# Kernel optimization log

Measured on AMD Instinct MI355X. Metric: run time of the kernel, lower is better.

The kernel has to match this reference:

```python
import jax, jax.numpy as jnp
import numpy as np

IN, H = 512, 1024
EPS = 1e-5

def _ln(x, g, b):
    mu = jnp.mean(x, axis=-1, keepdims=True)
    var = jnp.mean(jnp.square(x - mu), axis=-1, keepdims=True)
    return (x - mu) * jax.lax.rsqrt(var + EPS) * g + b

def setup_inputs() -> dict:
    key = jax.random.key(0)
    ks = jax.random.split(key, 8)
    B = 8192
    x = jax.random.normal(ks[0], (B, IN), jnp.float32)
    h_prev = jax.random.normal(ks[1], (B, H), jnp.float32)
    c_prev = jax.random.normal(ks[2], (B, H), jnp.float32)
    # Xavier-uniform weights (torch Linear: weight [out, in])
    lim_i = float(np.sqrt(6.0 / (IN + 4 * H)))
    lim_h = float(np.sqrt(6.0 / (H + 4 * H)))
    Wi = jax.random.uniform(ks[3], (4 * H, IN), jnp.float32, -lim_i, lim_i)
    Wh = jax.random.uniform(ks[4], (4 * H, H), jnp.float32, -lim_h, lim_h)
    # biases zero-ish with forget-gate slice set to 1.0 (matches _initialize_weights)
    bi = jnp.zeros((4 * H,), jnp.float32).at[H:2 * H].set(1.0)
    bh = jnp.zeros((4 * H,), jnp.float32).at[H:2 * H].set(1.0)
    g_in = jnp.ones((4 * H,), jnp.float32); b_in = jnp.zeros((4 * H,), jnp.float32)
    g_hid = jnp.ones((4 * H,), jnp.float32); b_hid = jnp.zeros((4 * H,), jnp.float32)
    g_cell = jnp.ones((H,), jnp.float32); b_cell = jnp.zeros((H,), jnp.float32)
    return {"x": x, "h_prev": h_prev, "c_prev": c_prev,
            "Wi": Wi, "bi": bi, "Wh": Wh, "bh": bh,
            "g_in": g_in, "b_in": b_in, "g_hid": g_hid, "b_hid": b_hid,
            "g_cell": g_cell, "b_cell": b_cell}

def reference(x, h_prev, c_prev, Wi, bi, Wh, bh, g_in, b_in, g_hid, b_hid, g_cell, b_cell):
    input_proj = _ln(x @ Wi.T + bi, g_in, b_in)          # [B, 4H]
    hidden_proj = _ln(h_prev @ Wh.T + bh, g_hid, b_hid)  # [B, 4H]
    combined = input_proj + hidden_proj
    i, f, g, o = jnp.split(combined, 4, axis=1)
    i = jax.nn.sigmoid(i); f = jax.nn.sigmoid(f)
    g = jnp.tanh(g); o = jax.nn.sigmoid(o)
    c_new = f * c_prev + i * g
    h_new = o * jnp.tanh(_ln(c_new, g_cell, b_cell))
    return (h_new, c_new)
```

## Files before the change

kernel.cpp:

```cpp
#include <hip/hip_runtime.h>
#include <hip/hip_bf16.h>

#define EPS 1e-5f

typedef __attribute__((ext_vector_type(8))) short short8;
typedef __attribute__((ext_vector_type(4))) short short4v;
typedef __attribute__((ext_vector_type(4))) float floatx4;

__device__ inline float b2f(short s) {
    union { unsigned u; float f; } v;
    v.u = ((unsigned)(unsigned short)s) << 16;
    return v.f;
}
__device__ inline float sigmoidf_(float x) { return 1.f / (1.f + __expf(-x)); }
__device__ inline float tanhf_(float x) { return 1.f - 2.f / (__expf(2.f * x) + 1.f); }

__device__ inline void load_lds16(const void* g, void* l) {
    __builtin_amdgcn_global_load_lds(
        (const __attribute__((address_space(1))) void*)g,
        (__attribute__((address_space(3))) void*)l, 16, 0, 0);
}

__global__ __launch_bounds__(256)
void cvt_bf16(const float* __restrict__ s0, __hip_bfloat16* __restrict__ d0, int n0_,
              const float* __restrict__ s1, __hip_bfloat16* __restrict__ d1, int n1_,
              const float* __restrict__ s2, __hip_bfloat16* __restrict__ d2, int n2_,
              const float* __restrict__ s3, __hip_bfloat16* __restrict__ d3, int n3_) {
    const float* s; __hip_bfloat16* d; int n;
    switch (blockIdx.y) {
        case 0:  s = s0; d = d0; n = n0_; break;
        case 1:  s = s1; d = d1; n = n1_; break;
        case 2:  s = s2; d = d2; n = n2_; break;
        default: s = s3; d = d3; n = n3_; break;
    }
    const int idx = (blockIdx.x * 256 + threadIdx.x) * 4;
    if (idx < n) {
        float4 v = *(const float4*)(s + idx);
        union { short4v sv; __hip_bfloat16 h[4]; } u;
        u.h[0] = __float2bfloat16(v.x); u.h[1] = __float2bfloat16(v.y);
        u.h[2] = __float2bfloat16(v.z); u.h[3] = __float2bfloat16(v.w);
        *(short4v*)(d + idx) = u.sv;
    }
}

__global__ __launch_bounds__(256, 3)
void gemm_bf16(const __hip_bfloat16* __restrict__ A, const __hip_bfloat16* __restrict__ W,
               const float* __restrict__ bias, __hip_bfloat16* __restrict__ out, int K) {
    __shared__ alignas(16) __hip_bfloat16 smem[17408];
    __hip_bfloat16* sA = smem;
    __hip_bfloat16* sB = smem + 8192;

    const int t    = threadIdx.x;
    const int lane = t & 63;
    const int wave = t >> 6;
    const int quad = lane >> 4;
    const int rl   = lane & 15;
    const int wm   = (wave >> 1) * 64;
    const int wn   = (wave & 1) * 64;
    const int m0   = blockIdx.y * 128;
    const int n0   = blockIdx.x * 128;

    floatx4 acc[4][4];
    #pragma unroll
    for (int i = 0; i < 4; ++i)
        #pragma unroll
        for (int j = 0; j < 4; ++j)
            acc[i][j] = (floatx4){0.f, 0.f, 0.f, 0.f};

    int srow[4], scol[4];
    #pragma unroll
    for (int i = 0; i < 4; ++i) {
        const int cl  = (wave * 4 + i) * 64 + lane;
        const int row = cl >> 3;
        srow[i] = row;
        scol[i] = ((cl & 7) ^ (row & 7)) * 8;
    }

    for (int k0 = 0; k0 < K; k0 += 64) {
        __syncthreads();
        #pragma unroll
        for (int i = 0; i < 4; ++i) {
            load_lds16(A + (size_t)(m0 + srow[i]) * K + k0 + scol[i], sA + (wave * 4 + i) * 512);
            load_lds16(W + (size_t)(n0 + srow[i]) * K + k0 + scol[i], sB + (wave * 4 + i) * 512);
        }
        __syncthreads();
        #pragma unroll
        for (int kk = 0; kk < 2; ++kk) {
            short8 aF[4], bF[4];
            #pragma unroll
            for (int i = 0; i < 4; ++i) {
                const int r = wm + i * 16 + rl;
                const int c = kk * 4 + quad;
                aF[i] = *(const short8*)(sA + (r * 8 + (c ^ (r & 7))) * 8);
            }
            #pragma unroll
            for (int j = 0; j < 4; ++j) {
                const int r = wn + j * 16 + rl;
                const int c = kk * 4 + quad;
                bF[j] = *(const short8*)(sB + (r * 8 + (c ^ (r & 7))) * 8);
            }
            #pragma unroll
            for (int i = 0; i < 4; ++i)
                #pragma unroll
                for (int j = 0; j < 4; ++j)
                    acc[i][j] = __builtin_amdgcn_mfma_f32_16x16x32_bf16(aF[i], bF[j], acc[i][j], 0, 0, 0);
        }
    }

    __syncthreads();
    #pragma unroll
    for (int j = 0; j < 4; ++j) {
        const int col = wn + j * 16 + rl;
        const float bv = bias[n0 + col];
        #pragma unroll
        for (int i = 0; i < 4; ++i) {
            const int rbase = wm + i * 16 + quad * 4;
            #pragma unroll
            for (int r = 0; r < 4; ++r)
                smem[(rbase + r) * 136 + col] = __float2bfloat16(acc[i][j][r] + bv);
        }
    }
    __syncthreads();
    #pragma unroll
    for (int p = 0; p < 8; ++p) {
        const int ch  = p * 256 + t;
        const int row = ch >> 4;
        const int c8  = (ch & 15) * 8;
        short8 v = *(const short8*)(smem + row * 136 + c8);
        *(short8*)(out + (size_t)(m0 + row) * 4096 + n0 + c8) = v;
    }
}

__device__ inline void red4(float& a, float& b, float& c, float& d, float* sred) {
    #pragma unroll
    for (int off = 32; off > 0; off >>= 1) {
        a += __shfl_down(a, off); b += __shfl_down(b, off);
        c += __shfl_down(c, off); d += __shfl_down(d, off);
    }
    const int w = threadIdx.x >> 6;
    if ((threadIdx.x & 63) == 0) {
        sred[w] = a; sred[w + 4] = b; sred[w + 8] = c; sred[w + 12] = d;
    }
    __syncthreads();
    a = sred[0] + sred[1] + sred[2] + sred[3];
    b = sred[4] + sred[5] + sred[6] + sred[7];
    c = sred[8] + sred[9] + sred[10] + sred[11];
    d = sred[12] + sred[13] + sred[14] + sred[15];
    __syncthreads();
}

__device__ inline void red2(float& a, float& b, float* sred) {
    #pragma unroll
    for (int off = 32; off > 0; off >>= 1) {
        a += __shfl_down(a, off); b += __shfl_down(b, off);
    }
    const int w = threadIdx.x >> 6;
    if ((threadIdx.x & 63) == 0) { sred[w] = a; sred[w + 4] = b; }
    __syncthreads();
    a = sred[0] + sred[1] + sred[2] + sred[3];
    b = sred[4] + sred[5] + sred[6] + sred[7];
    __syncthreads();
}

__global__ __launch_bounds__(256)
void ln_gates(const __hip_bfloat16* __restrict__ Pi, const __hip_bfloat16* __restrict__ Ph,
              const float* __restrict__ c_prev,
              const float* __restrict__ g_in, const float* __restrict__ b_in,
              const float* __restrict__ g_hid, const float* __restrict__ b_hid,
              const float* __restrict__ g_cell, const float* __restrict__ b_cell,
              float* __restrict__ h_out, float* __restrict__ c_out) {
    const int row = blockIdx.x;
    const int t   = threadIdx.x;
    __shared__ float sred[16];

    const __hip_bfloat16* pi = Pi + (size_t)row * 4096;
    const __hip_bfloat16* ph = Ph + (size_t)row * 4096;

    float si = 0.f, sqi = 0.f, sh = 0.f, sqh = 0.f;
    #pragma unroll
    for (int it = 0; it < 2; ++it) {
        const int s = t + it * 256;
        short8 vi = *(const short8*)(pi + s * 8);
        short8 vh = *(const short8*)(ph + s * 8);
        #pragma unroll
        for (int e = 0; e < 8; ++e) {
            float f = b2f(vi[e]); si += f; sqi += f * f;
            float g = b2f(vh[e]); sh += g; sqh += g * g;
        }
    }
    red4(si, sqi, sh, sqh, sred);
    const float mu_i = si * (1.f / 4096.f);
    const float rs_i = rsqrtf(sqi * (1.f / 4096.f) - mu_i * mu_i + EPS);
    const float mu_h = sh * (1.f / 4096.f);
    const float rs_h = rsqrtf(sqh * (1.f / 4096.f) - mu_h * mu_h + EPS);

    const int j0 = t * 4;
    float comb[4][4];
    #pragma unroll
    for (int gidx = 0; gidx < 4; ++gidx) {
        const int col = gidx * 1024 + j0;
        short4v vi = *(const short4v*)(pi + col);
        short4v vh = *(const short4v*)(ph + col);
        floatx4 gi  = *(const floatx4*)(g_in  + col);
        floatx4 bii = *(const floatx4*)(b_in  + col);
        floatx4 gh  = *(const floatx4*)(g_hid + col);
        floatx4 bhh = *(const floatx4*)(b_hid + col);
        #pragma unroll
        for (int e = 0; e < 4; ++e)
            comb[gidx][e] = (b2f(vi[e]) - mu_i) * rs_i * gi[e] + bii[e]
                          + (b2f(vh[e]) - mu_h) * rs_h * gh[e] + bhh[e];
    }

    floatx4 cp = *(const floatx4*)(c_prev + (size_t)row * 1024 + j0);
    float cn[4], ov[4];
    float sc = 0.f, scq = 0.f;
    #pragma unroll
    for (int e = 0; e < 4; ++e) {
        const float iv = sigmoidf_(comb[0][e]);
        const float fv = sigmoidf_(comb[1][e]);
        const float gv = tanhf_(comb[2][e]);
        ov[e] = sigmoidf_(comb[3][e]);
        const float c = fv * cp[e] + iv * gv;
        cn[e] = c; sc += c; scq += c * c;
    }
    red2(sc, scq, sred);
    const float mu_c = sc * (1.f / 1024.f);
    const float rs_c = rsqrtf(scq * (1.f / 1024.f) - mu_c * mu_c + EPS);

    floatx4 gc = *(const floatx4*)(g_cell + j0);
    floatx4 bc = *(const floatx4*)(b_cell + j0);
    floatx4 hv, cv;
    #pragma unroll
    for (int e = 0; e < 4; ++e) {
        const float nc = (cn[e] - mu_c) * rs_c * gc[e] + bc[e];
        hv[e] = ov[e] * tanhf_(nc);
        cv[e] = cn[e];
    }
    *(floatx4*)(h_out + (size_t)row * 1024 + j0) = hv;
    *(floatx4*)(c_out + (size_t)row * 1024 + j0) = cv;
}

extern "C" void kernel_launch(void* const* d_in, const int* in_sizes, int n_in,
                              void* d_out, int out_size, void* d_ws, size_t ws_size,
                              hipStream_t stream) {
    const float* x      = (const float*)d_in[0];
    const float* h_prev = (const float*)d_in[1];
    const float* c_prev = (const float*)d_in[2];
    const float* Wi     = (const float*)d_in[3];
    const float* bi     = (const float*)d_in[4];
    const float* Wh     = (const float*)d_in[5];
    const float* bh     = (const float*)d_in[6];
    const float* g_in   = (const float*)d_in[7];
    const float* b_in   = (const float*)d_in[8];
    const float* g_hid  = (const float*)d_in[9];
    const float* b_hid  = (const float*)d_in[10];
    const float* g_cell = (const float*)d_in[11];
    const float* b_cell = (const float*)d_in[12];

    __hip_bfloat16* Pi = (__hip_bfloat16*)d_ws;
    __hip_bfloat16* Ph = Pi + (size_t)8192 * 4096;

    const int NX = 8192 * 512, NH = 8192 * 1024, NWI = 4096 * 512, NWH = 4096 * 1024;
    __hip_bfloat16* xb  = (__hip_bfloat16*)d_out;
    __hip_bfloat16* hb  = xb + NX;
    __hip_bfloat16* Wib = hb + NH;
    __hip_bfloat16* Whb = Wib + NWI;

    float* h_out = (float*)d_out;
    float* c_out = h_out + (size_t)8192 * 1024;

    hipLaunchKernelGGL(cvt_bf16, dim3(8192, 4), dim3(256), 0, stream,
                       x, xb, NX, h_prev, hb, NH, Wi, Wib, NWI, Wh, Whb, NWH);

    dim3 grid(32, 64), blk(256);
    hipLaunchKernelGGL(gemm_bf16, grid, blk, 0, stream, xb, Wib, bi, Pi, 512);
    hipLaunchKernelGGL(gemm_bf16, grid, blk, 0, stream, hb, Whb, bh, Ph, 1024);
    hipLaunchKernelGGL(ln_gates, dim3(8192), blk, 0, stream, Pi, Ph, c_prev,
                       g_in, b_in, g_hid, b_hid, g_cell, b_cell, h_out, c_out);
}
```

Baseline: 340.6 us.

## Fuse LayerNorm row statistics into GEMM epilogue to skip a reduction pass

The GEMM epilogue now computes per-row partial sums and sums of squares of the biased outputs in fp32, reduces them across lanes, and writes 64 partials per row to workspace. A new ln_gates_fast kernel reads those partials instead of re-reading the full 4096-wide bf16 projections to compute mean and variance, so each row's projections are read once instead of twice. This adds shuffles and small stat stores to the GEMM epilogue. The path is only taken when the workspace is large enough, otherwise it falls back to the old kernel.

```diff
diff --git a/kernel.cpp b/kernel.cpp
--- a/kernel.cpp
+++ b/kernel.cpp
@@ -45,7 +45,8 @@
 
 __global__ __launch_bounds__(256, 3)
 void gemm_bf16(const __hip_bfloat16* __restrict__ A, const __hip_bfloat16* __restrict__ W,
-               const float* __restrict__ bias, __hip_bfloat16* __restrict__ out, int K) {
+               const float* __restrict__ bias, __hip_bfloat16* __restrict__ out,
+               float* __restrict__ sumOut, float* __restrict__ sqOut, int K) {
     __shared__ alignas(16) __hip_bfloat16 smem[17408];
     __hip_bfloat16* sA = smem;
     __hip_bfloat16* sB = smem + 8192;
@@ -59,6 +60,7 @@
     const int wn   = (wave & 1) * 64;
     const int m0   = blockIdx.y * 128;
     const int n0   = blockIdx.x * 128;
+    const int bn   = blockIdx.x;
 
     floatx4 acc[4][4];
     #pragma unroll
@@ -108,16 +110,36 @@
     }
 
     __syncthreads();
-    #pragma unroll
-    for (int j = 0; j < 4; ++j) {
-        const int col = wn + j * 16 + rl;
-        const float bv = bias[n0 + col];
-        #pragma unroll
-        for (int i = 0; i < 4; ++i) {
-            const int rbase = wm + i * 16 + quad * 4;
+    const bool doStats = (sumOut != nullptr);
+    float bvr[4];
+    #pragma unroll
+    for (int j = 0; j < 4; ++j) bvr[j] = bias[n0 + wn + j * 16 + rl];
+
+    #pragma unroll
+    for (int i = 0; i < 4; ++i) {
+        #pragma unroll
+        for (int r = 0; r < 4; ++r) {
+            const int lrow = wm + i * 16 + quad * 4 + r;
+            float s = 0.f, q = 0.f;
             #pragma unroll
-            for (int r = 0; r < 4; ++r)
-                smem[(rbase + r) * 136 + col] = __float2bfloat16(acc[i][j][r] + bv);
+            for (int j = 0; j < 4; ++j) {
+                const float v = acc[i][j][r] + bvr[j];
+                smem[lrow * 136 + wn + j * 16 + rl] = __float2bfloat16(v);
+                s += v; q += v * v;
+            }
+            if (doStats) {
+                #pragma unroll
+                for (int mask = 1; mask <= 8; mask <<= 1) {
+                    s += __shfl_xor(s, mask);
+                    q += __shfl_xor(q, mask);
+                }
+                if (rl == 0) {
+                    const int grow = m0 + lrow;
+                    const int part = bn * 2 + (wave & 1);
+                    sumOut[(size_t)grow * 64 + part] = s;
+                    sqOut[(size_t)grow * 64 + part] = q;
+                }
+            }
         }
     }
     __syncthreads();
@@ -160,6 +182,88 @@
     a = sred[0] + sred[1] + sred[2] + sred[3];
     b = sred[4] + sred[5] + sred[6] + sred[7];
     __syncthreads();
+}
+
+__global__ __launch_bounds__(256)
+void ln_gates_fast(const __hip_bfloat16* __restrict__ Pi, const __hip_bfloat16* __restrict__ Ph,
+                   const float* __restrict__ c_prev,
+                   const float* __restrict__ sPi, const float* __restrict__ qPi,
+                   const float* __restrict__ sPh, const float* __restrict__ qPh,
+                   const float* __restrict__ g_in, const float* __restrict__ b_in,
+                   const float* __restrict__ g_hid, const float* __restrict__ b_hid,
+                   const float* __restrict__ g_cell, const float* __restrict__ b_cell,
+                   float* __restrict__ h_out, float* __restrict__ c_out) {
+    const int row  = blockIdx.x;
+    const int t    = threadIdx.x;
+    const int lane = t & 63;
+    __shared__ float sred[16];
+
+    const __hip_bfloat16* pi = Pi + (size_t)row * 4096;
+    const __hip_bfloat16* ph = Ph + (size_t)row * 4096;
+    const int j0 = t * 4;
+
+    short4v piv[4], phv[4];
+    #pragma unroll
+    for (int g = 0; g < 4; ++g) {
+        piv[g] = *(const short4v*)(pi + g * 1024 + j0);
+        phv[g] = *(const short4v*)(ph + g * 1024 + j0);
+    }
+    floatx4 cp = *(const floatx4*)(c_prev + (size_t)row * 1024 + j0);
+
+    float a = sPi[(size_t)row * 64 + lane];
+    float b = qPi[(size_t)row * 64 + lane];
+    float c = sPh[(size_t)row * 64 + lane];
+    float d = qPh[(size_t)row * 64 + lane];
+    #pragma unroll
+    for (int mask = 1; mask <= 32; mask <<= 1) {
+        a += __shfl_xor(a, mask); b += __shfl_xor(b, mask);
+        c += __shfl_xor(c, mask); d += __shfl_xor(d, mask);
+    }
+    const float mu_i = a * (1.f / 4096.f);
+    const float rs_i = rsqrtf(b * (1.f / 4096.f) - mu_i * mu_i + EPS);
+    const float mu_h = c * (1.f / 4096.f);
+    const float rs_h = rsqrtf(d * (1.f / 4096.f) - mu_h * mu_h + EPS);
+
+    float comb[4][4];
+    #pragma unroll
+    for (int g = 0; g < 4; ++g) {
+        const int col = g * 1024 + j0;
+        floatx4 gi  = *(const floatx4*)(g_in  + col);
+        floatx4 bii = *(const floatx4*)(b_in  + col);
+        floatx4 gh  = *(const floatx4*)(g_hid + col);
+        floatx4 bhh = *(const floatx4*)(b_hid + col);
+        #pragma unroll
+        for (int e = 0; e < 4; ++e)
+            comb[g][e] = (b2f(piv[g][e]) - mu_i) * rs_i * gi[e] + bii[e]
+                       + (b2f(phv[g][e]) - mu_h) * rs_h * gh[e] + bhh[e];
+    }
+
+    float cn[4], ov[4];
+    float sc = 0.f, scq = 0.f;
+    #pragma unroll
+    for (int e = 0; e < 4; ++e) {
+        const float iv = sigmoidf_(comb[0][e]);
+        const float fv = sigmoidf_(comb[1][e]);
+        const float gv = tanhf_(comb[2][e]);
+        ov[e] = sigmoidf_(comb[3][e]);
+        const float cc = fv * cp[e] + iv * gv;
+        cn[e] = cc; sc += cc; scq += cc * cc;
+    }
+    red2(sc, scq, sred);
+    const float mu_c = sc * (1.f / 1024.f);
+    const float rs_c = rsqrtf(scq * (1.f / 1024.f) - mu_c * mu_c + EPS);
+
+    floatx4 gc = *(const floatx4*)(g_cell + j0);
+    floatx4 bc = *(const floatx4*)(b_cell + j0);
+    floatx4 hv, cv;
+    #pragma unroll
+    for (int e = 0; e < 4; ++e) {
+        const float nc = (cn[e] - mu_c) * rs_c * gc[e] + bc[e];
+        hv[e] = ov[e] * tanhf_(nc);
+        cv[e] = cn[e];
+    }
+    *(floatx4*)(h_out + (size_t)row * 1024 + j0) = hv;
+    *(floatx4*)(c_out + (size_t)row * 1024 + j0) = cv;
 }
 
 __global__ __launch_bounds__(256)
@@ -197,8 +301,8 @@
     const int j0 = t * 4;
     float comb[4][4];
     #pragma unroll
-    for (int gidx = 0; gidx < 4; ++gidx) {
-        const int col = gidx * 1024 + j0;
+    for (int g = 0; g < 4; ++g) {
+        const int col = g * 1024 + j0;
         short4v vi = *(const short4v*)(pi + col);
         short4v vh = *(const short4v*)(ph + col);
         floatx4 gi  = *(const floatx4*)(g_in  + col);
@@ -207,8 +311,8 @@
         floatx4 bhh = *(const floatx4*)(b_hid + col);
         #pragma unroll
         for (int e = 0; e < 4; ++e)
-            comb[gidx][e] = (b2f(vi[e]) - mu_i) * rs_i * gi[e] + bii[e]
-                          + (b2f(vh[e]) - mu_h) * rs_h * gh[e] + bhh[e];
+            comb[g][e] = (b2f(vi[e]) - mu_i) * rs_i * gi[e] + bii[e]
+                       + (b2f(vh[e]) - mu_h) * rs_h * gh[e] + bhh[e];
     }
 
     floatx4 cp = *(const floatx4*)(c_prev + (size_t)row * 1024 + j0);
@@ -260,6 +364,16 @@
     __hip_bfloat16* Pi = (__hip_bfloat16*)d_ws;
     __hip_bfloat16* Ph = Pi + (size_t)8192 * 4096;
 
+    const size_t base    = (size_t)2 * 8192 * 4096 * sizeof(__hip_bfloat16);
+    const size_t statN   = (size_t)8192 * 64;
+    const size_t need    = base + 4 * statN * sizeof(float);
+    const bool   fast    = (ws_size >= need);
+
+    float* sPi = (float*)((char*)d_ws + base);
+    float* qPi = sPi + statN;
+    float* sPh = qPi + statN;
+    float* qPh = sPh + statN;
+
     const int NX = 8192 * 512, NH = 8192 * 1024, NWI = 4096 * 512, NWH = 4096 * 1024;
     __hip_bfloat16* xb  = (__hip_bfloat16*)d_out;
     __hip_bfloat16* hb  = xb + NX;
@@ -273,8 +387,16 @@
                        x, xb, NX, h_prev, hb, NH, Wi, Wib, NWI, Wh, Whb, NWH);
 
     dim3 grid(32, 64), blk(256);
-    hipLaunchKernelGGL(gemm_bf16, grid, blk, 0, stream, xb, Wib, bi, Pi, 512);
-    hipLaunchKernelGGL(gemm_bf16, grid, blk, 0, stream, hb, Whb, bh, Ph, 1024);
-    hipLaunchKernelGGL(ln_gates, dim3(8192), blk, 0, stream, Pi, Ph, c_prev,
-                       g_in, b_in, g_hid, b_hid, g_cell, b_cell, h_out, c_out);
-}
+    hipLaunchKernelGGL(gemm_bf16, grid, blk, 0, stream, xb, Wib, bi, Pi,
+                       fast ? sPi : nullptr, fast ? qPi : nullptr, 512);
+    hipLaunchKernelGGL(gemm_bf16, grid, blk, 0, stream, hb, Whb, bh, Ph,
+                       fast ? sPh : nullptr, fast ? qPh : nullptr, 1024);
+    if (fast) {
+        hipLaunchKernelGGL(ln_gates_fast, dim3(8192), blk, 0, stream, Pi, Ph, c_prev,
+                           sPi, qPi, sPh, qPh,
+                           g_in, b_in, g_hid, b_hid, g_cell, b_cell, h_out, c_out);
+    } else {
+        hipLaunchKernelGGL(ln_gates, dim3(8192), blk, 0, stream, Pi, Ph, c_prev,
+                           g_in, b_in, g_hid, b_hid, g_cell, b_cell, h_out, c_out);
+    }
+}
```

Result: slower. 365.3 us (+7.3%).
